# Kernel tuning notes

Measured on AMD Instinct MI355X. Metric: run time of the kernel, lower is better.

Reference implementation:

```python
import jax, jax.numpy as jnp
import numpy as np

B, S, D = 2, 2048, 1024
H, HD = 16, 64          # n_heads, head_dim (H*HD == D)
E, K, F = 8, 2, 1024    # n_experts, top_k, expert hidden size
EPS = 1e-6


def setup_inputs() -> dict:
    key = jax.random.key(0)
    ks = jax.random.split(key, 10)
    g = lambda k, shape, sc: jax.random.normal(k, shape, jnp.float32) * sc
    return {
        "x": g(ks[0], (B, S, D), 1.0),
        "attn_norm_w": jnp.ones((D,), jnp.float32),
        "wq": g(ks[1], (D, D), 0.02),
        "wk": g(ks[2], (D, D), 0.02),
        "wv": g(ks[3], (D, D), 0.02),
        "wo": g(ks[4], (D, D), 0.02),
        "ffn_norm_w": jnp.ones((D,), jnp.float32),
        "router_w": g(ks[5], (D, E), 0.02),
        "w1": g(ks[6], (E, D, F), 0.02),  # gate proj per expert
        "w3": g(ks[7], (E, D, F), 0.02),  # up proj per expert
        "w2": g(ks[8], (E, F, D), 0.02),  # down proj per expert
    }


def rmsnorm(x, w):
    return x * jax.lax.rsqrt(jnp.mean(x * x, axis=-1, keepdims=True) + EPS) * w


def attention(x, wq, wk, wv, wo):
    b, s, d = x.shape
    q = (x @ wq).reshape(b, s, H, HD)
    k = (x @ wk).reshape(b, s, H, HD)
    v = (x @ wv).reshape(b, s, H, HD)
    scores = jnp.einsum("bqhd,bkhd->bhqk", q, k) / jnp.sqrt(jnp.float32(HD))
    causal = jnp.tril(jnp.ones((s, s), bool))
    scores = jnp.where(causal, scores, jnp.finfo(scores.dtype).min)
    p = jax.nn.softmax(scores, axis=-1)
    o = jnp.einsum("bhqk,bkhd->bqhd", p, v).reshape(b, s, d)
    return o @ wo


def moe_ffn(x, router_w, w1, w2, w3):
    b, s, d = x.shape
    xt = x.reshape(-1, d)                       # [T, D]
    probs = jax.nn.softmax(xt @ router_w, axis=-1)  # [T, E]
    gate, idx = jax.lax.top_k(probs, K)         # [T, K]
    gate = gate / jnp.sum(gate, axis=-1, keepdims=True)  # renormalize top-k
    T = xt.shape[0]
    combine = jnp.zeros((T, E), xt.dtype).at[jnp.arange(T)[:, None], idx].set(gate)
    out = jnp.zeros_like(xt)
    for e in range(E):  # fixed small loop over experts (dense-equivalent dispatch)
        h = jax.nn.silu(xt @ w1[e]) * (xt @ w3[e])
        out = out + combine[:, e:e + 1] * (h @ w2[e])
    return out.reshape(b, s, d)


def reference(x, attn_norm_w, wq, wk, wv, wo, ffn_norm_w, router_w, w1, w2, w3):
    # h = x + dropout(attn(norm(x)));  out = h + dropout(moe(norm(h)))  (dropout=0)
    h = x + attention(rmsnorm(x, attn_norm_w), wq, wk, wv, wo)
    return h + moe_ffn(rmsnorm(h, ffn_norm_w), router_w, w1, w2, w3)
```

## Files before the change

kernel.cpp:

```cpp
#include <hip/hip_runtime.h>
#include <cstdint>
#include <math.h>

typedef unsigned short u16;
typedef unsigned int u32;
typedef __bf16 bf16x8 __attribute__((ext_vector_type(8)));
typedef float f32x4 __attribute__((ext_vector_type(4)));

#define TBATCH 2
#define TSEQ   2048
#define TDIM   1024
#define THEADS 16
#define THDIM  64
#define TEXP   8
#define TFF    1024
#define TTOK   (TBATCH*TSEQ)
#define TPAIRS (TTOK*2)

__device__ __forceinline__ u16 f2bf(float f) {
  u32 u = __float_as_uint(f);
  u += 0x7FFFu + ((u >> 16) & 1u);
  return (u16)(u >> 16);
}
__device__ __forceinline__ float bf2f(u16 h) { return __uint_as_float(((u32)h) << 16); }

__device__ __forceinline__ void gll16(const void* g, void* l) {
  __builtin_amdgcn_global_load_lds((const __attribute__((address_space(1))) void*)g,
                                   (__attribute__((address_space(3))) void*)l, 16, 0, 0);
}
__device__ __forceinline__ bf16x8 ldsread(const void* p) { return *(const bf16x8*)p; }
__device__ __forceinline__ f32x4 mm16(bf16x8 a, bf16x8 b, f32x4 c) {
  return __builtin_amdgcn_mfma_f32_16x16x32_bf16(a, b, c, 0, 0, 0);
}
__device__ __forceinline__ f32x4 fzero() { f32x4 z = {0.f, 0.f, 0.f, 0.f}; return z; }

__global__ void split_transpose_k(const float* __restrict__ in, u16* __restrict__ outh,
                                  u16* __restrict__ outl, int R, int C) {
  __shared__ float t[32][33];
  const size_t bo = (size_t)blockIdx.z * R * C;
  const int c0 = blockIdx.x * 32, r0 = blockIdx.y * 32;
  const int tx = threadIdx.x, ty = threadIdx.y;
#pragma unroll
  for (int j = 0; j < 32; j += 8)
    t[ty + j][tx] = in[bo + (size_t)(r0 + ty + j) * C + (c0 + tx)];
  __syncthreads();
#pragma unroll
  for (int j = 0; j < 32; j += 8) {
    float v = t[tx][ty + j];
    u16 hv = f2bf(v);
    size_t o = bo + (size_t)(c0 + ty + j) * R + (r0 + tx);
    outh[o] = hv;
    if (outl != nullptr) outl[o] = f2bf(v - bf2f(hv));
  }
}

template<bool SPLIT>
__launch_bounds__(256)
__global__ void rmsnorm_k(const float* __restrict__ x, const float* __restrict__ w,
                          u16* __restrict__ oh, u16* __restrict__ ol) {
  const int t = blockIdx.x, tid = threadIdx.x;
  const float4 xv = ((const float4*)(x + (size_t)t * TDIM))[tid];
  float ss = xv.x*xv.x + xv.y*xv.y + xv.z*xv.z + xv.w*xv.w;
#pragma unroll
  for (int d = 1; d < 64; d <<= 1) ss += __shfl_xor(ss, d, 64);
  __shared__ float sp[4];
  if ((tid & 63) == 0) sp[tid >> 6] = ss;
  __syncthreads();
  const float rsc = rsqrtf((sp[0] + sp[1] + sp[2] + sp[3]) * (1.0f / TDIM) + 1e-6f);
  const float4 wv = ((const float4*)w)[tid];
  float v0 = xv.x*rsc*wv.x, v1 = xv.y*rsc*wv.y, v2 = xv.z*rsc*wv.z, v3 = xv.w*rsc*wv.w;
  u16 h0 = f2bf(v0), h1 = f2bf(v1), h2 = f2bf(v2), h3 = f2bf(v3);
  uint2 ph; ph.x = (u32)h0 | ((u32)h1 << 16); ph.y = (u32)h2 | ((u32)h3 << 16);
  *(uint2*)(oh + (size_t)t * TDIM + tid * 4) = ph;
  if (SPLIT) {
    u16 l0 = f2bf(v0 - bf2f(h0)), l1 = f2bf(v1 - bf2f(h1));
    u16 l2 = f2bf(v2 - bf2f(h2)), l3 = f2bf(v3 - bf2f(h3));
    uint2 pl; pl.x = (u32)l0 | ((u32)l1 << 16); pl.y = (u32)l2 | ((u32)l3 << 16);
    *(uint2*)(ol + (size_t)t * TDIM + tid * 4) = pl;
  }
}

template<int EPI>
__launch_bounds__(256)
__global__ void gemm_x3_k(const u16* __restrict__ Ah, const u16* __restrict__ Al,
                          const u16* __restrict__ Bth, const u16* __restrict__ Btl,
                          u16* __restrict__ outh, u16* __restrict__ outl,
                          float* __restrict__ outf, const float* __restrict__ resid,
                          int M, int N, int K) {
  __shared__ u16 sAh[128 * 32], sAl[128 * 32], sBh[64 * 32], sBl[64 * 32];
  const int tid = threadIdx.x, wid = tid >> 6, lane = tid & 63;
  const int m0 = blockIdx.x * 128, n0 = blockIdx.y * 64;
  const int wr = wid >> 1, wc = wid & 1;

  f32x4 acc[4][2];
#pragma unroll
  for (int i = 0; i < 4; i++)
#pragma unroll
    for (int j = 0; j < 2; j++) acc[i][j] = fzero();

  const int srow = tid >> 2;
  const int scol = (tid & 3) * 8;
  const size_t a0 = (size_t)(m0 + srow) * K + scol;
  const size_t a1 = (size_t)(m0 + srow + 64) * K + scol;
  const size_t b0 = (size_t)(n0 + srow) * K + scol;
  const int ldsw = wid * 1024;

  int aoffs[4], boffs[2];
#pragma unroll
  for (int mf = 0; mf < 4; mf++) aoffs[mf] = (wr*64 + mf*16 + (lane & 15)) * 64 + ((lane >> 4) * 16);
#pragma unroll
  for (int nf = 0; nf < 2; nf++) boffs[nf] = (wc*32 + nf*16 + (lane & 15)) * 64 + ((lane >> 4) * 16);

  const int nk = K >> 5;
  for (int kk = 0; kk < nk; ++kk) {
    const int ke = kk * 32;
    gll16(Ah + a0 + ke, (char*)sAh + ldsw);
    gll16(Ah + a1 + ke, (char*)sAh + 4096 + ldsw);
    gll16(Al + a0 + ke, (char*)sAl + ldsw);
    gll16(Al + a1 + ke, (char*)sAl + 4096 + ldsw);
    gll16(Bth + b0 + ke, (char*)sBh + ldsw);
    gll16(Btl + b0 + ke, (char*)sBl + ldsw);
    __syncthreads();
    bf16x8 fah[4], fal[4], fbh[2], fbl[2];
#pragma unroll
    for (int mf = 0; mf < 4; mf++) { fah[mf] = ldsread((char*)sAh + aoffs[mf]); fal[mf] = ldsread((char*)sAl + aoffs[mf]); }
#pragma unroll
    for (int nf = 0; nf < 2; nf++) { fbh[nf] = ldsread((char*)sBh + boffs[nf]); fbl[nf] = ldsread((char*)sBl + boffs[nf]); }
#pragma unroll
    for (int mf = 0; mf < 4; mf++)
#pragma unroll
      for (int nf = 0; nf < 2; nf++) {
        acc[mf][nf] = mm16(fah[mf], fbh[nf], acc[mf][nf]);
        acc[mf][nf] = mm16(fah[mf], fbl[nf], acc[mf][nf]);
        acc[mf][nf] = mm16(fal[mf], fbh[nf], acc[mf][nf]);
      }
    __syncthreads();
  }

#pragma unroll
  for (int mf = 0; mf < 4; mf++)
#pragma unroll
    for (int nf = 0; nf < 2; nf++)
#pragma unroll
      for (int r = 0; r < 4; r++) {
        const int grow = m0 + wr*64 + mf*16 + ((lane >> 4) * 4) + r;
        const int gcol = n0 + wc*32 + nf*16 + (lane & 15);
        const float v = acc[mf][nf][r];
        if (EPI == 0) {
          const size_t o = (size_t)grow * N + gcol;
          u16 hv = f2bf(v);
          outh[o] = hv; outl[o] = f2bf(v - bf2f(hv));
        } else if (EPI == 1) {
          const int b = grow >> 11, s = grow & (TSEQ - 1);
          const int hh = gcol >> 6, hd = gcol & 63;
          const size_t o = ((size_t)((b * THEADS + hh) * THDIM + hd)) * TSEQ + s;
          u16 hv = f2bf(v);
          outh[o] = hv; outl[o] = f2bf(v - bf2f(hv));
        } else {
          const size_t o = (size_t)grow * N + gcol;
          outf[o] = v + resid[o];
        }
      }
}

__launch_bounds__(256)
__global__ void flash_k(const u16* __restrict__ Qh, const u16* __restrict__ Ql,
                        const u16* __restrict__ Kh, const u16* __restrict__ Kl,
                        const u16* __restrict__ Vth, const u16* __restrict__ Vtl,
                        u16* __restrict__ Oh, u16* __restrict__ Ol) {
  __shared__ u16 sKh[64 * 64], sKl[64 * 64], sVh[64 * 64], sVl[64 * 64];
  __shared__ u16 sPh[4][16 * 64], sPl[4][16 * 64];
  const int tid = threadIdx.x, wid = tid >> 6, lane = tid & 63;
  const int qb = blockIdx.x, bh = blockIdx.y;
  const int b = bh >> 4, h = bh & 15;
  const int srow = tid >> 3;
  const int scol = (tid & 7) * 8;
  const int ldsw = wid * 1024;

  const size_t q0 = ((size_t)(b * TSEQ + qb * 64 + srow)) * TDIM + h * 64 + scol;
  const size_t q1 = q0 + (size_t)32 * TDIM;
  gll16(Qh + q0, (char*)sKh + ldsw);
  gll16(Qh + q1, (char*)sKh + 4096 + ldsw);
  __syncthreads();
  const int aoffQ = (wid * 16 + (lane & 15)) * 128 + ((lane >> 4) * 16);
  bf16x8 fqh[2], fql[2];
  fqh[0] = ldsread((char*)sKh + aoffQ);
  fqh[1] = ldsread((char*)sKh + aoffQ + 64);
  __syncthreads();
  gll16(Ql + q0, (char*)sKh + ldsw);
  gll16(Ql + q1, (char*)sKh + 4096 + ldsw);
  __syncthreads();
  fql[0] = ldsread((char*)sKh + aoffQ);
  fql[1] = ldsread((char*)sKh + aoffQ + 64);
  __syncthreads();

  f32x4 oacc[4];
  float m_run[4], l_run[4];
#pragma unroll
  for (int i = 0; i < 4; i++) { oacc[i] = fzero(); m_run[i] = -INFINITY; l_run[i] = 0.f; }

  const size_t k0 = ((size_t)(b * TSEQ + srow)) * TDIM + h * 64 + scol;
  const size_t k1 = k0 + (size_t)32 * TDIM;
  const size_t v0 = ((size_t)((b * THEADS + h) * THDIM + srow)) * TSEQ + scol;
  const size_t v1 = v0 + (size_t)32 * TSEQ;

  for (int kb = 0; kb <= qb; ++kb) {
    const size_t ko = (size_t)kb * 64 * TDIM;
    const size_t vo = (size_t)kb * 64;
    gll16(Kh + k0 + ko, (char*)sKh + ldsw);
    gll16(Kh + k1 + ko, (char*)sKh + 4096 + ldsw);
    gll16(Kl + k0 + ko, (char*)sKl + ldsw);
    gll16(Kl + k1 + ko, (char*)sKl + 4096 + ldsw);
    gll16(Vth + v0 + vo, (char*)sVh + ldsw);
    gll16(Vth + v1 + vo, (char*)sVh + 4096 + ldsw);
    gll16(Vtl + v0 + vo, (char*)sVl + ldsw);
    gll16(Vtl + v1 + vo, (char*)sVl + 4096 + ldsw);
    __syncthreads();

    f32x4 sc[4];
#pragma unroll
    for (int nf = 0; nf < 4; nf++) {
      f32x4 s = fzero();
#pragma unroll
      for (int kq = 0; kq < 2; kq++) {
        const int bo = (nf * 16 + (lane & 15)) * 128 + kq * 64 + ((lane >> 4) * 16);
        bf16x8 kfh = ldsread((char*)sKh + bo);
        bf16x8 kfl = ldsread((char*)sKl + bo);
        s = mm16(fqh[kq], kfh, s);
        s = mm16(fqh[kq], kfl, s);
        s = mm16(fql[kq], kfh, s);
      }
      sc[nf] = s;
    }

    const int qg = qb * 64 + wid * 16 + ((lane >> 4) * 4);
    float pm[4] = {-INFINITY, -INFINITY, -INFINITY, -INFINITY};
#pragma unroll
    for (int nf = 0; nf < 4; nf++) {
      const int kg = kb * 64 + nf * 16 + (lane & 15);
#pragma unroll
      for (int r = 0; r < 4; r++) {
        float v = sc[nf][r] * 0.125f;
        if (kg > qg + r) v = -INFINITY;
        sc[nf][r] = v;
        pm[r] = fmaxf(pm[r], v);
      }
    }
#pragma unroll
    for (int r = 0; r < 4; r++)
#pragma unroll
      for (int d = 1; d < 16; d <<= 1) pm[r] = fmaxf(pm[r], __shfl_xor(pm[r], d, 64));

    float mn[4], esc[4], rs[4];
#pragma unroll
    for (int r = 0; r < 4; r++) {
      mn[r] = fmaxf(m_run[r], pm[r]);
      esc[r] = __expf(m_run[r] - mn[r]);
      rs[r] = 0.f;
    }
#pragma unroll
    for (int nf = 0; nf < 4; nf++)
#pragma unroll
      for (int r = 0; r < 4; r++) {
        float p = __expf(sc[nf][r] - mn[r]);
        sc[nf][r] = p;
        rs[r] += p;
      }
#pragma unroll
    for (int r = 0; r < 4; r++)
#pragma unroll
      for (int d = 1; d < 16; d <<= 1) rs[r] += __shfl_xor(rs[r], d, 64);
#pragma unroll
    for (int r = 0; r < 4; r++) {
      l_run[r] = l_run[r] * esc[r] + rs[r];
      m_run[r] = mn[r];
    }
#pragma unroll
    for (int nf = 0; nf < 4; nf++)
#pragma unroll
      for (int r = 0; r < 4; r++) oacc[nf][r] *= esc[r];

#pragma unroll
    for (int nf = 0; nf < 4; nf++)
#pragma unroll
      for (int r = 0; r < 4; r++) {
        float p = sc[nf][r];
        u16 ph = f2bf(p);
        const int idx = (((lane >> 4) * 4) + r) * 64 + nf * 16 + (lane & 15);
        sPh[wid][idx] = ph;
        sPl[wid][idx] = f2bf(p - bf2f(ph));
      }
    __syncthreads();

#pragma unroll
    for (int nf = 0; nf < 4; nf++) {
#pragma unroll
      for (int kq = 0; kq < 2; kq++) {
        const int po = (lane & 15) * 128 + kq * 64 + ((lane >> 4) * 16);
        bf16x8 pah = ldsread((char*)sPh[wid] + po);
        bf16x8 pal = ldsread((char*)sPl[wid] + po);
        const int voff = (nf * 16 + (lane & 15)) * 128 + kq * 64 + ((lane >> 4) * 16);
        bf16x8 vfh = ldsread((char*)sVh + voff);
        bf16x8 vfl = ldsread((char*)sVl + voff);
        oacc[nf] = mm16(pah, vfh, oacc[nf]);
        oacc[nf] = mm16(pah, vfl, oacc[nf]);
        oacc[nf] = mm16(pal, vfh, oacc[nf]);
      }
    }
    __syncthreads();
  }

#pragma unroll
  for (int r = 0; r < 4; r++) {
    const float inv = 1.0f / l_run[r];
    const int t = b * TSEQ + qb * 64 + wid * 16 + ((lane >> 4) * 4) + r;
#pragma unroll
    for (int nf = 0; nf < 4; nf++) {
      const float v = oacc[nf][r] * inv;
      const size_t o = (size_t)t * TDIM + h * 64 + nf * 16 + (lane & 15);
      u16 hv = f2bf(v);
      Oh[o] = hv; Ol[o] = f2bf(v - bf2f(hv));
    }
  }
}

__launch_bounds__(256)
__global__ void router_k(const float* __restrict__ hres, const float* __restrict__ wn,
                         const float* __restrict__ rw, int* __restrict__ idx01,
                         float* __restrict__ gate01, int* __restrict__ counts) {
  const int t = blockIdx.x, tid = threadIdx.x;
  const float4 xv = ((const float4*)(hres + (size_t)t * TDIM))[tid];
  float ss = xv.x*xv.x + xv.y*xv.y + xv.z*xv.z + xv.w*xv.w;
#pragma unroll
  for (int d = 1; d < 64; d <<= 1) ss += __shfl_xor(ss, d, 64);
  __shared__ float sp[4];
  __shared__ float sacc[4][8];
  if ((tid & 63) == 0) sp[tid >> 6] = ss;
  __syncthreads();
  const float rsc = rsqrtf((sp[0]+sp[1]+sp[2]+sp[3]) * (1.0f / TDIM) + 1e-6f);
  const float4 wv = ((const float4*)wn)[tid];
  const float x0 = xv.x*rsc*wv.x, x1 = xv.y*rsc*wv.y, x2 = xv.z*rsc*wv.z, x3 = xv.w*rsc*wv.w;
  const float* rp = rw + (size_t)(tid * 4) * TEXP;
  float acc[8];
#pragma unroll
  for (int e = 0; e < 8; e++) acc[e] = x0*rp[e] + x1*rp[8+e] + x2*rp[16+e] + x3*rp[24+e];
#pragma unroll
  for (int e = 0; e < 8; e++)
#pragma unroll
    for (int d = 1; d < 64; d <<= 1) acc[e] += __shfl_xor(acc[e], d, 64);
  if ((tid & 63) == 0)
#pragma unroll
    for (int e = 0; e < 8; e++) sacc[tid >> 6][e] = acc[e];
  __syncthreads();
  if (tid == 0) {
    float lg[8];
#pragma unroll
    for (int e = 0; e < 8; e++) lg[e] = sacc[0][e] + sacc[1][e] + sacc[2][e] + sacc[3][e];
    int i1 = 0;
#pragma unroll
    for (int e = 1; e < 8; e++) if (lg[e] > lg[i1]) i1 = e;
    int i2 = (i1 == 0) ? 1 : 0;
#pragma unroll
    for (int e = 0; e < 8; e++) if (e != i1 && lg[e] > lg[i2]) i2 = e;
    const float g1 = 1.0f / (1.0f + __expf(lg[i2] - lg[i1]));
    idx01[t*2] = i1; idx01[t*2+1] = i2;
    gate01[t*2] = g1; gate01[t*2+1] = 1.0f - g1;
    atomicAdd(&counts[i1], 1);
    atomicAdd(&counts[i2], 1);
  }
}

__global__ void zero8_k(int* counts) { if (threadIdx.x < TEXP) counts[threadIdx.x] = 0; }

__global__ void offsets_k(const int* __restrict__ counts, int* __restrict__ cursor,
                          int* __restrict__ bm_e, int* __restrict__ bm_s0,
                          int* __restrict__ bm_end, int* __restrict__ n_active) {
  if (threadIdx.x != 0 || blockIdx.x != 0) return;
  int off = 0, nb = 0;
  for (int e = 0; e < TEXP; e++) {
    const int c = counts[e];
    cursor[e] = off;
    const int end = off + c;
    for (int mb = 0; mb * 128 < c; mb++) { bm_e[nb] = e; bm_s0[nb] = off + mb * 128; bm_end[nb] = end; nb++; }
    off = end;
  }
  *n_active = nb;
}

__global__ void scatter_k(const int* __restrict__ idx01, int* __restrict__ cursor,
                          int* __restrict__ slot_of, int* __restrict__ perm) {
  const int t = blockIdx.x * 256 + threadIdx.x;
  if (t >= TTOK) return;
#pragma unroll
  for (int k = 0; k < 2; k++) {
    const int e = idx01[t*2+k];
    const int slot = atomicAdd(&cursor[e], 1);
    slot_of[t*2+k] = slot;
    perm[slot] = t;
  }
}

__launch_bounds__(256)
__global__ void moe_gemm1_k(const u16* __restrict__ hn, const u16* __restrict__ w1t,
                            const u16* __restrict__ w3t, const int* __restrict__ perm,
                            const int* __restrict__ bm_e, const int* __restrict__ bm_s0,
                            const int* __restrict__ bm_end, const int* __restrict__ n_active,
                            u16* __restrict__ hbuf) {
  if ((int)blockIdx.x >= *n_active) return;
  __shared__ u16 sA[128 * 32], sB1[64 * 32], sB3[64 * 32];
  const int tid = threadIdx.x, wid = tid >> 6, lane = tid & 63;
  const int e = bm_e[blockIdx.x], slot0 = bm_s0[blockIdx.x], send = bm_end[blockIdx.x];
  const int n0 = blockIdx.y * 64;
  const int wr = wid >> 1, wc = wid & 1;
  const int srow = tid >> 2, scol = (tid & 3) * 8;
  const int sa0 = slot0 + srow, sa1 = slot0 + srow + 64;
  const int ta = (sa0 < send) ? perm[sa0] : 0;
  const int tb2 = (sa1 < send) ? perm[sa1] : 0;
  const size_t a0 = (size_t)ta * TDIM + scol;
  const size_t a1 = (size_t)tb2 * TDIM + scol;
  const size_t bb = (size_t)e * TDIM * TFF + (size_t)(n0 + srow) * TDIM + scol;
  const int ldsw = wid * 1024;
  f32x4 ac1[4][2], ac3[4][2];
#pragma unroll
  for (int i = 0; i < 4; i++)
#pragma unroll
    for (int j = 0; j < 2; j++) { ac1[i][j] = fzero(); ac3[i][j] = fzero(); }
  int aoffs[4], boffs[2];
#pragma unroll
  for (int mf = 0; mf < 4; mf++) aoffs[mf] = (wr*64 + mf*16 + (lane & 15)) * 64 + ((lane >> 4) * 16);
#pragma unroll
  for (int nf = 0; nf < 2; nf++) boffs[nf] = (wc*32 + nf*16 + (lane & 15)) * 64 + ((lane >> 4) * 16);

  for (int kk = 0; kk < 32; ++kk) {
    const int ke = kk * 32;
    gll16(hn + a0 + ke, (char*)sA + ldsw);
    gll16(hn + a1 + ke, (char*)sA + 4096 + ldsw);
    gll16(w1t + bb + ke, (char*)sB1 + ldsw);
    gll16(w3t + bb + ke, (char*)sB3 + ldsw);
    __syncthreads();
    bf16x8 fa[4], f1[2], f3[2];
#pragma unroll
    for (int mf = 0; mf < 4; mf++) fa[mf] = ldsread((char*)sA + aoffs[mf]);
#pragma unroll
    for (int nf = 0; nf < 2; nf++) { f1[nf] = ldsread((char*)sB1 + boffs[nf]); f3[nf] = ldsread((char*)sB3 + boffs[nf]); }
#pragma unroll
    for (int mf = 0; mf < 4; mf++)
#pragma unroll
      for (int nf = 0; nf < 2; nf++) {
        ac1[mf][nf] = mm16(fa[mf], f1[nf], ac1[mf][nf]);
        ac3[mf][nf] = mm16(fa[mf], f3[nf], ac3[mf][nf]);
      }
    __syncthreads();
  }

#pragma unroll
  for (int mf = 0; mf < 4; mf++)
#pragma unroll
    for (int nf = 0; nf < 2; nf++)
#pragma unroll
      for (int r = 0; r < 4; r++) {
        const int slot = slot0 + wr*64 + mf*16 + ((lane >> 4) * 4) + r;
        if (slot < send) {
          const int col = n0 + wc*32 + nf*16 + (lane & 15);
          const float z1 = ac1[mf][nf][r], z3 = ac3[mf][nf][r];
          const float hv = z1 / (1.0f + __expf(-z1)) * z3;
          hbuf[(size_t)slot * TFF + col] = f2bf(hv);
        }
      }
}

__launch_bounds__(256)
__global__ void moe_gemm2_k(const u16* __restrict__ hbuf, const u16* __restrict__ w2t,
                            const int* __restrict__ bm_e, const int* __restrict__ bm_s0,
                            const int* __restrict__ bm_end, const int* __restrict__ n_active,
                            u16* __restrict__ pout) {
  if ((int)blockIdx.x >= *n_active) return;
  __shared__ u16 sA[128 * 32], sB[64 * 32];
  const int tid = threadIdx.x, wid = tid >> 6, lane = tid & 63;
  const int e = bm_e[blockIdx.x], slot0 = bm_s0[blockIdx.x], send = bm_end[blockIdx.x];
  const int n0 = blockIdx.y * 64;
  const int wr = wid >> 1, wc = wid & 1;
  const int srow = tid >> 2, scol = (tid & 3) * 8;
  int sa0 = slot0 + srow; if (sa0 > TPAIRS - 1) sa0 = TPAIRS - 1;
  int sa1 = slot0 + srow + 64; if (sa1 > TPAIRS - 1) sa1 = TPAIRS - 1;
  const size_t a0 = (size_t)sa0 * TFF + scol;
  const size_t a1 = (size_t)sa1 * TFF + scol;
  const size_t bb = (size_t)e * TDIM * TFF + (size_t)(n0 + srow) * TFF + scol;
  const int ldsw = wid * 1024;
  f32x4 acc[4][2];
#pragma unroll
  for (int i = 0; i < 4; i++)
#pragma unroll
    for (int j = 0; j < 2; j++) acc[i][j] = fzero();
  int aoffs[4], boffs[2];
#pragma unroll
  for (int mf = 0; mf < 4; mf++) aoffs[mf] = (wr*64 + mf*16 + (lane & 15)) * 64 + ((lane >> 4) * 16);
#pragma unroll
  for (int nf = 0; nf < 2; nf++) boffs[nf] = (wc*32 + nf*16 + (lane & 15)) * 64 + ((lane >> 4) * 16);

  for (int kk = 0; kk < 32; ++kk) {
    const int ke = kk * 32;
    gll16(hbuf + a0 + ke, (char*)sA + ldsw);
    gll16(hbuf + a1 + ke, (char*)sA + 4096 + ldsw);
    gll16(w2t + bb + ke, (char*)sB + ldsw);
    __syncthreads();
    bf16x8 fa[4], fb[2];
#pragma unroll
    for (int mf = 0; mf < 4; mf++) fa[mf] = ldsread((char*)sA + aoffs[mf]);
#pragma unroll
    for (int nf = 0; nf < 2; nf++) fb[nf] = ldsread((char*)sB + boffs[nf]);
#pragma unroll
    for (int mf = 0; mf < 4; mf++)
#pragma unroll
      for (int nf = 0; nf < 2; nf++)
        acc[mf][nf] = mm16(fa[mf], fb[nf], acc[mf][nf]);
    __syncthreads();
  }

#pragma unroll
  for (int mf = 0; mf < 4; mf++)
#pragma unroll
    for (int nf = 0; nf < 2; nf++)
#pragma unroll
      for (int r = 0; r < 4; r++) {
        const int slot = slot0 + wr*64 + mf*16 + ((lane >> 4) * 4) + r;
        if (slot < send) {
          const int col = n0 + wc*32 + nf*16 + (lane & 15);
          pout[(size_t)slot * TDIM + col] = f2bf(acc[mf][nf][r]);
        }
      }
}

__launch_bounds__(256)
__global__ void combine_k(const float* __restrict__ hres, const u16* __restrict__ pout,
                          const int* __restrict__ slot_of, const float* __restrict__ gate01,
                          float* __restrict__ out) {
  const int t = blockIdx.x, tid = threadIdx.x;
  const int s0 = slot_of[t*2], s1 = slot_of[t*2+1];
  const float g0 = gate01[t*2], g1 = gate01[t*2+1];
  const float4 hv = ((const float4*)(hres + (size_t)t * TDIM))[tid];
  const uint2 u0 = *(const uint2*)(pout + (size_t)s0 * TDIM + tid * 4);
  const uint2 u1 = *(const uint2*)(pout + (size_t)s1 * TDIM + tid * 4);
  float4 o;
  o.x = hv.x + g0 * bf2f((u16)(u0.x & 0xffff)) + g1 * bf2f((u16)(u1.x & 0xffff));
  o.y = hv.y + g0 * bf2f((u16)(u0.x >> 16))    + g1 * bf2f((u16)(u1.x >> 16));
  o.z = hv.z + g0 * bf2f((u16)(u0.y & 0xffff)) + g1 * bf2f((u16)(u1.y & 0xffff));
  o.w = hv.w + g0 * bf2f((u16)(u0.y >> 16))    + g1 * bf2f((u16)(u1.y >> 16));
  ((float4*)(out + (size_t)t * TDIM))[tid] = o;
}

extern "C" void kernel_launch(void* const* d_in, const int* in_sizes, int n_in,
                              void* d_out, int out_size, void* d_ws, size_t ws_size,
                              hipStream_t stream) {
  (void)in_sizes; (void)n_in; (void)out_size; (void)ws_size;
  const float* x   = (const float*)d_in[0];
  const float* anw = (const float*)d_in[1];
  const float* wq  = (const float*)d_in[2];
  const float* wk  = (const float*)d_in[3];
  const float* wv  = (const float*)d_in[4];
  const float* wo  = (const float*)d_in[5];
  const float* fnw = (const float*)d_in[6];
  const float* rw  = (const float*)d_in[7];
  const float* w1  = (const float*)d_in[8];
  const float* w3  = (const float*)d_in[9];
  const float* w2  = (const float*)d_in[10];
  float* out = (float*)d_out;

  char* ws = (char*)d_ws;
  size_t off = 0;
  auto take = [&](size_t bytes) -> char* {
    char* p = ws + off;
    off += (bytes + 255) & ~(size_t)255;
    return p;
  };
  const size_t SZ_W = (size_t)TDIM * TDIM * sizeof(u16);
  const size_t SZ_T = (size_t)TTOK * TDIM * sizeof(u16);
  u16* wqt_h = (u16*)take(SZ_W); u16* wqt_l = (u16*)take(SZ_W);
  u16* wkt_h = (u16*)take(SZ_W); u16* wkt_l = (u16*)take(SZ_W);
  u16* wvt_h = (u16*)take(SZ_W); u16* wvt_l = (u16*)take(SZ_W);
  u16* wot_h = (u16*)take(SZ_W); u16* wot_l = (u16*)take(SZ_W);
  u16* w1t = (u16*)take((size_t)TEXP * TDIM * TFF * sizeof(u16));
  u16* w3t = (u16*)take((size_t)TEXP * TDIM * TFF * sizeof(u16));
  u16* w2t = (u16*)take((size_t)TEXP * TDIM * TFF * sizeof(u16));
  u16* xnh = (u16*)take(SZ_T); u16* xnl = (u16*)take(SZ_T);
  u16* qh  = (u16*)take(SZ_T); u16* ql  = (u16*)take(SZ_T);
  u16* kh  = (u16*)take(SZ_T); u16* kl  = (u16*)take(SZ_T);
  u16* vth = (u16*)take(SZ_T); u16* vtl = (u16*)take(SZ_T);
  float* hres = (float*)take((size_t)TTOK * TDIM * sizeof(float));
  int*   idx01  = (int*)take(TTOK * 2 * 4);
  float* gate01 = (float*)take(TTOK * 2 * 4);
  int*   slot_of = (int*)take(TTOK * 2 * 4);
  int*   perm    = (int*)take(TPAIRS * 4);
  int*   counts  = (int*)take(256);
  int*   cursor  = (int*)take(256);
  int*   bm_e    = (int*)take(96 * 4);
  int*   bm_s0   = (int*)take(96 * 4);
  int*   bm_end  = (int*)take(96 * 4);
  int*   n_act   = (int*)take(256);
  u16* oh = xnh; u16* ol = xnl;
  u16* hn = qh;
  u16* hbuf = kh;
  u16* pout = vth;

  dim3 tb32(32, 8);
  split_transpose_k<<<dim3(32, 32, 1), tb32, 0, stream>>>(wq, wqt_h, wqt_l, TDIM, TDIM);
  split_transpose_k<<<dim3(32, 32, 1), tb32, 0, stream>>>(wk, wkt_h, wkt_l, TDIM, TDIM);
  split_transpose_k<<<dim3(32, 32, 1), tb32, 0, stream>>>(wv, wvt_h, wvt_l, TDIM, TDIM);
  split_transpose_k<<<dim3(32, 32, 1), tb32, 0, stream>>>(wo, wot_h, wot_l, TDIM, TDIM);
  split_transpose_k<<<dim3(32, 32, 8), tb32, 0, stream>>>(w1, w1t, nullptr, TDIM, TFF);
  split_transpose_k<<<dim3(32, 32, 8), tb32, 0, stream>>>(w3, w3t, nullptr, TDIM, TFF);
  split_transpose_k<<<dim3(32, 32, 8), tb32, 0, stream>>>(w2, w2t, nullptr, TFF, TDIM);
  zero8_k<<<1, 64, 0, stream>>>(counts);
  rmsnorm_k<true><<<TTOK, 256, 0, stream>>>(x, anw, xnh, xnl);
  gemm_x3_k<0><<<dim3(TTOK/128, TDIM/64), 256, 0, stream>>>(xnh, xnl, wqt_h, wqt_l, qh, ql, nullptr, nullptr, TTOK, TDIM, TDIM);
  gemm_x3_k<0><<<dim3(TTOK/128, TDIM/64), 256, 0, stream>>>(xnh, xnl, wkt_h, wkt_l, kh, kl, nullptr, nullptr, TTOK, TDIM, TDIM);
  gemm_x3_k<1><<<dim3(TTOK/128, TDIM/64), 256, 0, stream>>>(xnh, xnl, wvt_h, wvt_l, vth, vtl, nullptr, nullptr, TTOK, TDIM, TDIM);
  flash_k<<<dim3(TSEQ/64, TBATCH*THEADS), 256, 0, stream>>>(qh, ql, kh, kl, vth, vtl, oh, ol);
  gemm_x3_k<2><<<dim3(TTOK/128, TDIM/64), 256, 0, stream>>>(oh, ol, wot_h, wot_l, nullptr, nullptr, hres, x, TTOK, TDIM, TDIM);
  rmsnorm_k<false><<<TTOK, 256, 0, stream>>>(hres, fnw, hn, nullptr);
  router_k<<<TTOK, 256, 0, stream>>>(hres, fnw, rw, idx01, gate01, counts);
  offsets_k<<<1, 1, 0, stream>>>(counts, cursor, bm_e, bm_s0, bm_end, n_act);
  scatter_k<<<TTOK/256, 256, 0, stream>>>(idx01, cursor, slot_of, perm);
  moe_gemm1_k<<<dim3(72, TFF/64), 256, 0, stream>>>(hn, w1t, w3t, perm, bm_e, bm_s0, bm_end, n_act, hbuf);
  moe_gemm2_k<<<dim3(72, TDIM/64), 256, 0, stream>>>(hbuf, w2t, bm_e, bm_s0, bm_end, n_act, pout);
  combine_k<<<TTOK, 256, 0, stream>>>(hres, pout, slot_of, gate01, out);
}
```

Before: 710.1 us.

## Double-buffer K/V tiles, swizzle LDS layouts, and load Q directly in flash attention

The flash attention kernel now double-buffers the K and V tiles in LDS, prefetching the next key block while the current one is computed, so that global loads overlap with MFMA work. K/V and P shared-memory layouts use an XOR swizzle to reduce LDS bank conflicts. Q fragments are loaded straight from global memory into registers instead of being staged through LDS with barriers. The intra-iteration barrier before the PV product is dropped because P is per-wave, and LDS use doubles for K/V.

```diff
diff --git a/kernel.cpp b/kernel.cpp
--- a/kernel.cpp
+++ b/kernel.cpp
@@ -168,64 +168,67 @@
                         const u16* __restrict__ Kh, const u16* __restrict__ Kl,
                         const u16* __restrict__ Vth, const u16* __restrict__ Vtl,
                         u16* __restrict__ Oh, u16* __restrict__ Ol) {
-  __shared__ u16 sKh[64 * 64], sKl[64 * 64], sVh[64 * 64], sVl[64 * 64];
-  __shared__ u16 sPh[4][16 * 64], sPl[4][16 * 64];
+  __shared__ u16 sK[2][2][4096];
+  __shared__ u16 sV[2][2][4096];
+  __shared__ u16 sP[2][4][1024];
   const int tid = threadIdx.x, wid = tid >> 6, lane = tid & 63;
   const int qb = blockIdx.x, bh = blockIdx.y;
   const int b = bh >> 4, h = bh & 15;
   const int srow = tid >> 3;
-  const int scol = (tid & 7) * 8;
+  const int sxcol = (((lane & 7) ^ ((lane >> 3) & 7)) << 3);
   const int ldsw = wid * 1024;
 
-  const size_t q0 = ((size_t)(b * TSEQ + qb * 64 + srow)) * TDIM + h * 64 + scol;
-  const size_t q1 = q0 + (size_t)32 * TDIM;
-  gll16(Qh + q0, (char*)sKh + ldsw);
-  gll16(Qh + q1, (char*)sKh + 4096 + ldsw);
-  __syncthreads();
-  const int aoffQ = (wid * 16 + (lane & 15)) * 128 + ((lane >> 4) * 16);
   bf16x8 fqh[2], fql[2];
-  fqh[0] = ldsread((char*)sKh + aoffQ);
-  fqh[1] = ldsread((char*)sKh + aoffQ + 64);
-  __syncthreads();
-  gll16(Ql + q0, (char*)sKh + ldsw);
-  gll16(Ql + q1, (char*)sKh + 4096 + ldsw);
-  __syncthreads();
-  fql[0] = ldsread((char*)sKh + aoffQ);
-  fql[1] = ldsread((char*)sKh + aoffQ + 64);
-  __syncthreads();
+  {
+    const size_t qbase = ((size_t)(b * TSEQ + qb * 64 + wid * 16 + (lane & 15))) * TDIM + h * 64;
+#pragma unroll
+    for (int kq = 0; kq < 2; kq++) {
+      fqh[kq] = *(const bf16x8*)(Qh + qbase + (kq * 4 + (lane >> 4)) * 8);
+      fql[kq] = *(const bf16x8*)(Ql + qbase + (kq * 4 + (lane >> 4)) * 8);
+    }
+  }
 
   f32x4 oacc[4];
   float m_run[4], l_run[4];
 #pragma unroll
   for (int i = 0; i < 4; i++) { oacc[i] = fzero(); m_run[i] = -INFINITY; l_run[i] = 0.f; }
 
-  const size_t k0 = ((size_t)(b * TSEQ + srow)) * TDIM + h * 64 + scol;
-  const size_t k1 = k0 + (size_t)32 * TDIM;
-  const size_t v0 = ((size_t)((b * THEADS + h) * THDIM + srow)) * TSEQ + scol;
-  const size_t v1 = v0 + (size_t)32 * TSEQ;
-
-  for (int kb = 0; kb <= qb; ++kb) {
+  const size_t kg0 = ((size_t)(b * TSEQ + srow)) * TDIM + h * 64 + sxcol;
+  const size_t kg1 = kg0 + (size_t)32 * TDIM;
+  const size_t vg0 = ((size_t)((b * THEADS + h) * THDIM + srow)) * TSEQ + sxcol;
+  const size_t vg1 = vg0 + (size_t)32 * TSEQ;
+
+  auto stage = [&](int kb, int bi) {
     const size_t ko = (size_t)kb * 64 * TDIM;
     const size_t vo = (size_t)kb * 64;
-    gll16(Kh + k0 + ko, (char*)sKh + ldsw);
-    gll16(Kh + k1 + ko, (char*)sKh + 4096 + ldsw);
-    gll16(Kl + k0 + ko, (char*)sKl + ldsw);
-    gll16(Kl + k1 + ko, (char*)sKl + 4096 + ldsw);
-    gll16(Vth + v0 + vo, (char*)sVh + ldsw);
-    gll16(Vth + v1 + vo, (char*)sVh + 4096 + ldsw);
-    gll16(Vtl + v0 + vo, (char*)sVl + ldsw);
-    gll16(Vtl + v1 + vo, (char*)sVl + 4096 + ldsw);
-    __syncthreads();
+    gll16(Kh + kg0 + ko, (char*)sK[bi][0] + ldsw);
+    gll16(Kh + kg1 + ko, (char*)sK[bi][0] + 4096 + ldsw);
+    gll16(Kl + kg0 + ko, (char*)sK[bi][1] + ldsw);
+    gll16(Kl + kg1 + ko, (char*)sK[bi][1] + 4096 + ldsw);
+    gll16(Vth + vg0 + vo, (char*)sV[bi][0] + ldsw);
+    gll16(Vth + vg1 + vo, (char*)sV[bi][0] + 4096 + ldsw);
+    gll16(Vtl + vg0 + vo, (char*)sV[bi][1] + ldsw);
+    gll16(Vtl + vg1 + vo, (char*)sV[bi][1] + 4096 + ldsw);
+  };
+
+  stage(0, 0);
+  asm volatile("s_waitcnt vmcnt(0)" ::: "memory");
+  __builtin_amdgcn_s_barrier();
+
+  for (int kb = 0; kb <= qb; ++kb) {
+    const int cur = kb & 1;
+    if (kb < qb) stage(kb + 1, cur ^ 1);
 
     f32x4 sc[4];
 #pragma unroll
     for (int nf = 0; nf < 4; nf++) {
       f32x4 s = fzero();
+      const int krow = nf * 16 + (lane & 15);
 #pragma unroll
       for (int kq = 0; kq < 2; kq++) {
-        const int bo = (nf * 16 + (lane & 15)) * 128 + kq * 64 + ((lane >> 4) * 16);
-        bf16x8 kfh = ldsread((char*)sKh + bo);
-        bf16x8 kfl = ldsread((char*)sKl + bo);
+        const int off = krow * 128 + (((kq * 4 + (lane >> 4)) ^ (lane & 7)) << 4);
+        bf16x8 kfh = ldsread((char*)sK[cur][0] + off);
+        bf16x8 kfl = ldsread((char*)sK[cur][1] + off);
         s = mm16(fqh[kq], kfh, s);
         s = mm16(fqh[kq], kfl, s);
         s = mm16(fql[kq], kfh, s);
@@ -286,28 +289,31 @@
       for (int r = 0; r < 4; r++) {
         float p = sc[nf][r];
         u16 ph = f2bf(p);
-        const int idx = (((lane >> 4) * 4) + r) * 64 + nf * 16 + (lane & 15);
-        sPh[wid][idx] = ph;
-        sPl[wid][idx] = f2bf(p - bf2f(ph));
-      }
-    __syncthreads();
+        const int prow = (lane >> 4) * 4 + r;
+        const int pbyte = (prow * 128 + (nf * 16 + (lane & 15)) * 2) ^ ((prow & 7) << 4);
+        *(u16*)((char*)sP[0][wid] + pbyte) = ph;
+        *(u16*)((char*)sP[1][wid] + pbyte) = f2bf(p - bf2f(ph));
+      }
 
 #pragma unroll
     for (int nf = 0; nf < 4; nf++) {
 #pragma unroll
       for (int kq = 0; kq < 2; kq++) {
-        const int po = (lane & 15) * 128 + kq * 64 + ((lane >> 4) * 16);
-        bf16x8 pah = ldsread((char*)sPh[wid] + po);
-        bf16x8 pal = ldsread((char*)sPl[wid] + po);
-        const int voff = (nf * 16 + (lane & 15)) * 128 + kq * 64 + ((lane >> 4) * 16);
-        bf16x8 vfh = ldsread((char*)sVh + voff);
-        bf16x8 vfl = ldsread((char*)sVl + voff);
+        const int prow = lane & 15;
+        const int poff = prow * 128 + (((kq * 4 + (lane >> 4)) ^ (prow & 7)) << 4);
+        bf16x8 pah = ldsread((char*)sP[0][wid] + poff);
+        bf16x8 pal = ldsread((char*)sP[1][wid] + poff);
+        const int vrow = nf * 16 + (lane & 15);
+        const int voff = vrow * 128 + (((kq * 4 + (lane >> 4)) ^ (lane & 7)) << 4);
+        bf16x8 vfh = ldsread((char*)sV[cur][0] + voff);
+        bf16x8 vfl = ldsread((char*)sV[cur][1] + voff);
         oacc[nf] = mm16(pah, vfh, oacc[nf]);
         oacc[nf] = mm16(pah, vfl, oacc[nf]);
         oacc[nf] = mm16(pal, vfh, oacc[nf]);
       }
     }
-    __syncthreads();
+    asm volatile("s_waitcnt vmcnt(0)" ::: "memory");
+    __builtin_amdgcn_s_barrier();
   }
 
 #pragma unroll
```

Measured after the change: 645.1 us. 9.2% less time.
